# Performance work log

Hardware: AMD Instinct MI355X
Metric: run time of the kernel (lower is better)

Reference implementation:

```python
import jax, jax.numpy as jnp
import numpy as np

B, T, H, S, K = 8, 1024, 8, 64, 31  # batch, time, heads, head_size, kernel_size
C = H * S


def setup_inputs() -> dict:
    key = jax.random.key(0)
    k1, k2, k3 = jax.random.split(key, 3)
    x = jax.random.normal(k1, (B, T, C), dtype=jnp.float32)
    filters = jax.random.normal(k2, (B, T, H * K), dtype=jnp.float32)
    bias = jax.random.normal(k3, (C,), dtype=jnp.float32) * 0.02
    return {"x": x, "filters": filters, "bias": bias}


def reference(x, filters, bias):
    # x: [B,T,C], filters: [B,T,H*K], bias: [C]
    pad = K // 2
    x_pad = jnp.pad(x, ((0, 0), (pad, pad), (0, 0)))  # [B, T+K-1, C]
    idx = jnp.arange(T)[:, None] + jnp.arange(K)[None, :]  # [T,K]
    win = x_pad[:, idx, :]                                  # [B,T,K,C]
    win = win.reshape(B, T, K, H, S)
    # softmax-normalized dynamic kernels per (b,t,h)
    w = jax.nn.softmax(filters.reshape(B, T, H, K), axis=-1)
    out = jnp.einsum('btkhs,bthk->bths', win, w).reshape(B, T, C)
    return out + bias[None, None, :]
```

## Files before the change

kernel.cpp:

```cpp
#include <hip/hip_runtime.h>


#define BB 8
#define TDIM 1024
#define HH 8
#define SS 64
#define KK 31
#define CC (HH * SS)
#define HK (HH * KK)
#define TTILE 64
#define WIN 96
#define PAD 15

__global__ __launch_bounds__(256, 2)
void lightconv_kernel(const float* __restrict__ xg,
                      const float* __restrict__ fg,
                      const float* __restrict__ bg,
                      float* __restrict__ og)
{
    __shared__ float xs[WIN * SS];
    __shared__ float ws[TTILE][32];

    const int t0  = blockIdx.x * TTILE;
    const int h   = blockIdx.y;
    const int b   = blockIdx.z;
    const int tid = threadIdx.x;

    {
        const float* xb = xg + ((size_t)b * TDIM) * CC + h * SS;
        #pragma unroll
        for (int i = 0; i < 6; ++i) {
            int f  = tid + i * 256;
            int r  = f >> 4;
            int c4 = (f & 15) << 2;
            int t  = t0 - PAD + r;
            float4 v = make_float4(0.f, 0.f, 0.f, 0.f);
            if ((unsigned)t < (unsigned)TDIM)
                v = *reinterpret_cast<const float4*>(xb + (size_t)t * CC + c4);
            *reinterpret_cast<float4*>(&xs[r * SS + c4]) = v;
        }
    }

    if (tid < TTILE) {
        const float* fp = fg + (size_t)(b * TDIM + t0 + tid) * HK + h * KK;
        float v[KK];
        float m = -1e30f;
        #pragma unroll
        for (int k = 0; k < KK; ++k) { v[k] = fp[k]; m = fmaxf(m, v[k]); }
        float s = 0.f;
        #pragma unroll
        for (int k = 0; k < KK; ++k) { v[k] = __expf(v[k] - m); s += v[k]; }
        float inv = 1.f / s;
        #pragma unroll
        for (int k = 0; k < KK; ++k) ws[tid][k] = v[k] * inv;
        ws[tid][KK] = 0.f;
    }
    __syncthreads();

    const int sq = (tid & 15) << 2;
    const int tb = (tid >> 4) << 2;

    float4 xw[35];
    #pragma unroll
    for (int j = 0; j < 35; ++j)
        xw[j] = *reinterpret_cast<const float4*>(&xs[(tb + j) * SS + sq]);

    float4 bias4 = *reinterpret_cast<const float4*>(bg + h * SS + sq);

    float4 acc[4];
    #pragma unroll
    for (int tt = 0; tt < 4; ++tt) acc[tt] = bias4;

    #pragma unroll
    for (int tt = 0; tt < 4; ++tt) {
        #pragma unroll
        for (int kq = 0; kq < 8; ++kq) {
            float4 w4 = *reinterpret_cast<const float4*>(&ws[tb + tt][kq << 2]);
            const float* wv = &w4.x;
            #pragma unroll
            for (int m = 0; m < 4; ++m) {
                float w = wv[m];
                float4 xv = xw[tt + (kq << 2) + m];
                acc[tt].x = fmaf(w, xv.x, acc[tt].x);
                acc[tt].y = fmaf(w, xv.y, acc[tt].y);
                acc[tt].z = fmaf(w, xv.z, acc[tt].z);
                acc[tt].w = fmaf(w, xv.w, acc[tt].w);
            }
        }
    }

    float* ob = og + (size_t)(b * TDIM + t0) * CC + h * SS;
    #pragma unroll
    for (int tt = 0; tt < 4; ++tt)
        *reinterpret_cast<float4*>(ob + (size_t)(tb + tt) * CC + sq) = acc[tt];
}

extern "C" void kernel_launch(void* const* d_in, const int* in_sizes, int n_in,
                              void* d_out, int out_size, void* d_ws, size_t ws_size,
                              hipStream_t stream)
{
    const float* x    = (const float*)d_in[0];
    const float* f    = (const float*)d_in[1];
    const float* bias = (const float*)d_in[2];
    float* out        = (float*)d_out;
    dim3 grid(TDIM / TTILE, HH, BB);
    lightconv_kernel<<<grid, 256, 0, stream>>>(x, f, bias, out);
}
```

Measured before the change: 82.25 us.

## Load x tiles directly to LDS and parallelize softmax across threads

Interior blocks now copy the x window into shared memory with direct global-to-LDS loads, skipping the trip through registers. Edge blocks keep the old zero-padded register path. The per-row softmax used to run on 64 threads, each reading all 31 filter values in turn. It now runs on all 256 threads, four per row, combining the max and sum with shuffles. The weight tile row stride is also padded to 36 to spread LDS bank accesses, at the cost of a little more shared memory and a branch that depends on the block position.

```diff
diff --git a/kernel.cpp b/kernel.cpp
--- a/kernel.cpp
+++ b/kernel.cpp
@@ -11,6 +11,7 @@
 #define TTILE 64
 #define WIN 96
 #define PAD 15
+#define WSTRIDE 36
 
 __global__ __launch_bounds__(256, 2)
 void lightconv_kernel(const float* __restrict__ xg,
@@ -19,15 +20,28 @@
                       float* __restrict__ og)
 {
     __shared__ float xs[WIN * SS];
-    __shared__ float ws[TTILE][32];
+    __shared__ float ws[TTILE * WSTRIDE];
 
     const int t0  = blockIdx.x * TTILE;
     const int h   = blockIdx.y;
     const int b   = blockIdx.z;
     const int tid = threadIdx.x;
 
-    {
-        const float* xb = xg + ((size_t)b * TDIM) * CC + h * SS;
+    const float* xb = xg + ((size_t)b * TDIM) * CC + h * SS;
+
+    if (blockIdx.x != 0 && blockIdx.x != (TDIM / TTILE - 1)) {
+        #pragma unroll
+        for (int i = 0; i < 6; ++i) {
+            int f  = tid + i * 256;
+            int r  = f >> 4;
+            int c4 = (f & 15) << 2;
+            const float* gp = xb + (size_t)(t0 - PAD + r) * CC + c4;
+            __builtin_amdgcn_global_load_lds(
+                (const __attribute__((address_space(1))) void*)gp,
+                (__attribute__((address_space(3))) void*)&xs[f << 2],
+                16, 0, 0);
+        }
+    } else {
         #pragma unroll
         for (int i = 0; i < 6; ++i) {
             int f  = tid + i * 256;
@@ -37,23 +51,34 @@
             float4 v = make_float4(0.f, 0.f, 0.f, 0.f);
             if ((unsigned)t < (unsigned)TDIM)
                 v = *reinterpret_cast<const float4*>(xb + (size_t)t * CC + c4);
-            *reinterpret_cast<float4*>(&xs[r * SS + c4]) = v;
+            *reinterpret_cast<float4*>(&xs[f << 2]) = v;
         }
     }
 
-    if (tid < TTILE) {
-        const float* fp = fg + (size_t)(b * TDIM + t0 + tid) * HK + h * KK;
-        float v[KK];
-        float m = -1e30f;
+    {
+        const int row  = tid >> 2;
+        const int q    = tid & 3;
+        const int base = q * 8;
+        const float* fp = fg + (size_t)(b * TDIM + t0 + row) * HK + h * KK + base;
+        float v[8];
         #pragma unroll
-        for (int k = 0; k < KK; ++k) { v[k] = fp[k]; m = fmaxf(m, v[k]); }
+        for (int j = 0; j < 8; ++j)
+            v[j] = (base + j < KK) ? fp[j] : -1e30f;
+        float m = v[0];
+        #pragma unroll
+        for (int j = 1; j < 8; ++j) m = fmaxf(m, v[j]);
+        m = fmaxf(m, __shfl_xor(m, 1, 4));
+        m = fmaxf(m, __shfl_xor(m, 2, 4));
         float s = 0.f;
         #pragma unroll
-        for (int k = 0; k < KK; ++k) { v[k] = __expf(v[k] - m); s += v[k]; }
+        for (int j = 0; j < 8; ++j) { v[j] = __expf(v[j] - m); s += v[j]; }
+        s += __shfl_xor(s, 1, 4);
+        s += __shfl_xor(s, 2, 4);
         float inv = 1.f / s;
         #pragma unroll
-        for (int k = 0; k < KK; ++k) ws[tid][k] = v[k] * inv;
-        ws[tid][KK] = 0.f;
+        for (int j = 0; j < 8; ++j)
+            if (base + j < 32)
+                ws[row * WSTRIDE + base + j] = v[j] * inv;
     }
     __syncthreads();
 
@@ -75,7 +100,7 @@
     for (int tt = 0; tt < 4; ++tt) {
         #pragma unroll
         for (int kq = 0; kq < 8; ++kq) {
-            float4 w4 = *reinterpret_cast<const float4*>(&ws[tb + tt][kq << 2]);
+            float4 w4 = *reinterpret_cast<const float4*>(&ws[(tb + tt) * WSTRIDE + (kq << 2)]);
             const float* wv = &w4.x;
             #pragma unroll
             for (int m = 0; m < 4; ++m) {
```

Result: no change. 81.55 us (-0.9%).
